# Kernel optimization log

Hardware: AMD Instinct MI355X
Metric: run time of the kernel (lower is better)

Reference implementation:

```python
import jax, jax.numpy as jnp
import numpy as np


def setup_inputs() -> dict:
    key = jax.random.key(0)
    x = jax.random.normal(key, (8, 192, 64, 64), dtype=jnp.float32)
    return {"x": x}


def reference(x):
    # x: [b, c, h, w]
    b, c, h, w = x.shape
    xf = x.reshape(b, c, h * w)                                   # [b, c, hw]
    # prepend global-mean token -> [b, c, T] with T = hw + 1
    xf = jnp.concatenate([xf.mean(axis=-1, keepdims=True), xf], axis=-1)
    scale = jnp.asarray(c, xf.dtype) ** -0.25                      # 1/sqrt(sqrt(c))
    qs = xf * scale
    # full T x T score matrix, as in the original module
    weight = jnp.einsum('bct,bcs->bts', qs, qs)                    # [b, T, T]
    weight = jax.nn.softmax(weight.astype(jnp.float32), axis=-1).astype(xf.dtype)
    out = jnp.einsum('bts,bcs->bct', weight, xf)                   # [b, c, T]
    return out[:, :, 0]                                            # [b, c]
```

## Files before the change

### kernel.cpp

```cpp
#include <hip/hip_runtime.h>

#define BB 8
#define CC 192
#define HWN 4096
#define SCALE2 0.07216878364870323f
#define NCHUNK 128
#define CW 32


#define GLOAD_LDS16(gp, lp)                                                    \
    __builtin_amdgcn_global_load_lds(                                          \
        (const __attribute__((address_space(1))) void*)(gp),                   \
        (__attribute__((address_space(3))) void*)(lp), 16, 0, 0)

__global__ void mean_kernel(const float* __restrict__ x, float* __restrict__ m) {
    int wave = threadIdx.x >> 6, lane = threadIdx.x & 63;
    int bc = blockIdx.x * 4 + wave;
    const float4* p4 = (const float4*)(x + (size_t)bc * HWN);
    float s = 0.f;
#pragma unroll
    for (int i = 0; i < 16; ++i) {
        float4 v = p4[lane + 64 * i];
        s += v.x + v.y + v.z + v.w;
    }
    for (int off = 32; off; off >>= 1) s += __shfl_down(s, off);
    if (lane == 0) m[bc] = s * (1.0f / HWN);
}

__global__ __launch_bounds__(256)
void fused_kernel(const float* __restrict__ x,
                  const float* __restrict__ m,
                  float* __restrict__ Zp,
                  float* __restrict__ Op) {
    const int chunk = blockIdx.x;
    const int b     = blockIdx.y;
    const int t     = threadIdx.x;

    __shared__ float tile[CC * CW];
    __shared__ float ml[CC];
    __shared__ float scp[256];
    __shared__ float wls[CW];

    const float* xb = x + (size_t)b * CC * HWN + chunk * CW;
#pragma unroll
    for (int it = 0; it < 6; ++it) {
        int i = t + it * 256;
        int c = i >> 3, k = i & 7;
        const float* gsrc = xb + (size_t)c * HWN + 4 * k;
        float* ldst = tile + 4 * (i & ~63);
        GLOAD_LDS16(gsrc, ldst);
    }
    if (t < CC) ml[t] = m[b * CC + t];
    __syncthreads();

    {
        int g = t >> 5, s = t & 31;
        int c0 = g * 24;
        float acc = 0.f;
#pragma unroll
        for (int c = 0; c < 24; ++c)
            acc += ml[c0 + c] * tile[(c0 + c) * CW + s];
        scp[t] = acc;
    }
    __syncthreads();

    if (t < CW) {
        float sc = 0.f;
#pragma unroll
        for (int g = 0; g < 8; ++g) sc += scp[g * 32 + t];
        float w = __expf(sc * SCALE2);
        wls[t] = w;
        float se = w;
        for (int off = 16; off; off >>= 1) se += __shfl_xor(se, off);
        if (t == 0) Zp[b * NCHUNK + chunk] = se;
    }
    __syncthreads();

    if (t < CC) {
        float o = 0.f;
#pragma unroll
        for (int j = 0; j < CW; ++j) {
            int s = (t + j) & (CW - 1);
            o += wls[s] * tile[t * CW + s];
        }
        Op[((size_t)b * NCHUNK + chunk) * CC + t] = o;
    }
}

__global__ __launch_bounds__(512)
void combine_kernel(const float* __restrict__ m,
                    const float* __restrict__ Zp,
                    const float* __restrict__ Op,
                    float* __restrict__ out) {
    int cg = blockIdx.x;
    int b  = blockIdx.y;
    int t  = threadIdx.x;
    __shared__ float psum[512];
    __shared__ float sInv, sE0;

    if (t < 64) {
        float z = Zp[b * NCHUNK + t] + Zp[b * NCHUNK + 64 + t];
        float q = m[b * CC + t] * m[b * CC + t]
                + m[b * CC + 64 + t] * m[b * CC + 64 + t]
                + m[b * CC + 128 + t] * m[b * CC + 128 + t];
        for (int off = 32; off; off >>= 1) {
            z += __shfl_xor(z, off);
            q += __shfl_xor(q, off);
        }
        if (t == 0) {
            float e0 = __expf(q * SCALE2);
            sE0 = e0;
            sInv = 1.0f / (z + e0);
        }
    }

    int grp = t >> 6;
    int c   = cg * 64 + (t & 63);
    const float* op = Op + ((size_t)b * NCHUNK + grp * 16) * CC + c;
    float acc = 0.f;
#pragma unroll
    for (int j = 0; j < 16; ++j)
        acc += op[(size_t)j * CC];
    psum[t] = acc;
    __syncthreads();

    if (t < 64) {
        float o = 0.f;
#pragma unroll
        for (int g = 0; g < 8; ++g)
            o += psum[g * 64 + t];
        int cc = cg * 64 + t;
        out[b * CC + cc] = (o + sE0 * m[b * CC + cc]) * sInv;
    }
}

extern "C" void kernel_launch(void* const* d_in, const int* in_sizes, int n_in,
                              void* d_out, int out_size, void* d_ws, size_t ws_size,
                              hipStream_t stream) {
    const float* x = (const float*)d_in[0];
    float* out = (float*)d_out;

    float* ws = (float*)d_ws;
    float* m  = ws;
    float* Zp = ws + 1536;
    float* Op = ws + 2560;

    mean_kernel<<<BB * CC / 4, 256, 0, stream>>>(x, m);
    fused_kernel<<<dim3(NCHUNK, BB), 256, 0, stream>>>(x, m, Zp, Op);
    combine_kernel<<<dim3(3, BB), 512, 0, stream>>>(m, Zp, Op, out);
}
```

Measured before the change: 18.84 us.

## Replace partial-sum buffers with atomic accumulation and simplify final normalization

Chunk blocks now atomically add their weighted channel sums and exp-sum directly into per-batch accumulators instead of writing per-chunk partials for a combine kernel to reduce. The mean kernel zeroes these accumulators and is relaunched with 256 blocks of 6 channels each, and the final kernel becomes a trivial divide. The output dot product is also vectorized to float4 LDS reads. This removes the Op write/read round trip and the combine reduction, at the cost of heavy atomic contention (128 chunks per address) and nondeterministic float summation order.

```diff
diff --git a/kernel.cpp b/kernel.cpp
--- a/kernel.cpp
+++ b/kernel.cpp
@@ -13,25 +13,33 @@
         (const __attribute__((address_space(1))) void*)(gp),                   \
         (__attribute__((address_space(3))) void*)(lp), 16, 0, 0)
 
-__global__ void mean_kernel(const float* __restrict__ x, float* __restrict__ m) {
-    int wave = threadIdx.x >> 6, lane = threadIdx.x & 63;
-    int bc = blockIdx.x * 4 + wave;
-    const float4* p4 = (const float4*)(x + (size_t)bc * HWN);
-    float s = 0.f;
+__global__ __launch_bounds__(256)
+void mean_kernel(const float* __restrict__ x, float* __restrict__ m,
+                 float* __restrict__ acc, float* __restrict__ Z) {
+    int blk = blockIdx.x;
+    int t   = threadIdx.x;
+    if (t < 6) acc[blk * 6 + t] = 0.f;
+    if (blk == 0 && t >= 8 && t < 16) Z[t - 8] = 0.f;
+    int wave = t >> 6, lane = t & 63;
+    for (int i = wave; i < 6; i += 4) {
+        int bc = blk * 6 + i;
+        const float4* p4 = (const float4*)(x + (size_t)bc * HWN);
+        float s = 0.f;
 #pragma unroll
-    for (int i = 0; i < 16; ++i) {
-        float4 v = p4[lane + 64 * i];
-        s += v.x + v.y + v.z + v.w;
+        for (int k = 0; k < 16; ++k) {
+            float4 v = p4[lane + 64 * k];
+            s += v.x + v.y + v.z + v.w;
+        }
+        for (int off = 32; off; off >>= 1) s += __shfl_down(s, off);
+        if (lane == 0) m[bc] = s * (1.0f / HWN);
     }
-    for (int off = 32; off; off >>= 1) s += __shfl_down(s, off);
-    if (lane == 0) m[bc] = s * (1.0f / HWN);
 }
 
 __global__ __launch_bounds__(256)
 void fused_kernel(const float* __restrict__ x,
                   const float* __restrict__ m,
-                  float* __restrict__ Zp,
-                  float* __restrict__ Op) {
+                  float* __restrict__ acc,
+                  float* __restrict__ Z) {
     const int chunk = blockIdx.x;
     const int b     = blockIdx.y;
     const int t     = threadIdx.x;
@@ -40,6 +48,7 @@
     __shared__ float ml[CC];
     __shared__ float scp[256];
     __shared__ float wls[CW];
+    __shared__ float sE0;
 
     const float* xb = x + (size_t)b * CC * HWN + chunk * CW;
 #pragma unroll
@@ -56,11 +65,11 @@
     {
         int g = t >> 5, s = t & 31;
         int c0 = g * 24;
-        float acc = 0.f;
+        float a = 0.f;
 #pragma unroll
         for (int c = 0; c < 24; ++c)
-            acc += ml[c0 + c] * tile[(c0 + c) * CW + s];
-        scp[t] = acc;
+            a += ml[c0 + c] * tile[(c0 + c) * CW + s];
+        scp[t] = a;
     }
     __syncthreads();
 
@@ -72,66 +81,42 @@
         wls[t] = w;
         float se = w;
         for (int off = 16; off; off >>= 1) se += __shfl_xor(se, off);
-        if (t == 0) Zp[b * NCHUNK + chunk] = se;
+        if (t == 0) atomicAdd(Z + b, se);
+    }
+    if (chunk == 0 && t >= 64 && t < 128) {
+        int u = t - 64;
+        float q = ml[u] * ml[u] + ml[64 + u] * ml[64 + u] + ml[128 + u] * ml[128 + u];
+        for (int off = 32; off; off >>= 1) q += __shfl_xor(q, off);
+        if (u == 0) {
+            float e0 = __expf(q * SCALE2);
+            sE0 = e0;
+            atomicAdd(Z + b, e0);
+        }
     }
     __syncthreads();
 
     if (t < CC) {
+        const float4* t4 = (const float4*)(tile + t * CW);
+        const float4* w4 = (const float4*)wls;
         float o = 0.f;
 #pragma unroll
-        for (int j = 0; j < CW; ++j) {
-            int s = (t + j) & (CW - 1);
-            o += wls[s] * tile[t * CW + s];
+        for (int j = 0; j < 8; ++j) {
+            int sg = (t + j) & 7;
+            float4 v = t4[sg];
+            float4 w = w4[sg];
+            o += v.x * w.x + v.y * w.y + v.z * w.z + v.w * w.w;
         }
-        Op[((size_t)b * NCHUNK + chunk) * CC + t] = o;
+        if (chunk == 0) o += sE0 * ml[t];
+        atomicAdd(acc + b * CC + t, o);
     }
 }
 
-__global__ __launch_bounds__(512)
-void combine_kernel(const float* __restrict__ m,
-                    const float* __restrict__ Zp,
-                    const float* __restrict__ Op,
-                    float* __restrict__ out) {
-    int cg = blockIdx.x;
-    int b  = blockIdx.y;
-    int t  = threadIdx.x;
-    __shared__ float psum[512];
-    __shared__ float sInv, sE0;
-
-    if (t < 64) {
-        float z = Zp[b * NCHUNK + t] + Zp[b * NCHUNK + 64 + t];
-        float q = m[b * CC + t] * m[b * CC + t]
-                + m[b * CC + 64 + t] * m[b * CC + 64 + t]
-                + m[b * CC + 128 + t] * m[b * CC + 128 + t];
-        for (int off = 32; off; off >>= 1) {
-            z += __shfl_xor(z, off);
-            q += __shfl_xor(q, off);
-        }
-        if (t == 0) {
-            float e0 = __expf(q * SCALE2);
-            sE0 = e0;
-            sInv = 1.0f / (z + e0);
-        }
-    }
-
-    int grp = t >> 6;
-    int c   = cg * 64 + (t & 63);
-    const float* op = Op + ((size_t)b * NCHUNK + grp * 16) * CC + c;
-    float acc = 0.f;
-#pragma unroll
-    for (int j = 0; j < 16; ++j)
-        acc += op[(size_t)j * CC];
-    psum[t] = acc;
-    __syncthreads();
-
-    if (t < 64) {
-        float o = 0.f;
-#pragma unroll
-        for (int g = 0; g < 8; ++g)
-            o += psum[g * 64 + t];
-        int cc = cg * 64 + t;
-        out[b * CC + cc] = (o + sE0 * m[b * CC + cc]) * sInv;
-    }
+__global__ __launch_bounds__(768)
+void norm_kernel(const float* __restrict__ acc, const float* __restrict__ Z,
+                 float* __restrict__ out) {
+    int i = blockIdx.x * 768 + threadIdx.x;
+    int b = i / CC;
+    out[i] = acc[i] / Z[b];
 }
 
 extern "C" void kernel_launch(void* const* d_in, const int* in_sizes, int n_in,
@@ -140,12 +125,12 @@
     const float* x = (const float*)d_in[0];
     float* out = (float*)d_out;
 
-    float* ws = (float*)d_ws;
-    float* m  = ws;
-    float* Zp = ws + 1536;
-    float* Op = ws + 2560;
+    float* ws  = (float*)d_ws;
+    float* m   = ws;
+    float* acc = ws + 1536;
+    float* Z   = ws + 3072;
 
-    mean_kernel<<<BB * CC / 4, 256, 0, stream>>>(x, m);
-    fused_kernel<<<dim3(NCHUNK, BB), 256, 0, stream>>>(x, m, Zp, Op);
-    combine_kernel<<<dim3(3, BB), 512, 0, stream>>>(m, Zp, Op, out);
+    mean_kernel<<<256, 256, 0, stream>>>(x, m, acc, Z);
+    fused_kernel<<<dim3(NCHUNK, BB), 256, 0, stream>>>(x, m, acc, Z);
+    norm_kernel<<<2, 768, 0, stream>>>(acc, Z, out);
 }
```

Result: slower. 29.10 us (+54.5%).
